# Kernel optimization log

Hardware: AMD Instinct MI355X
Metric: run time of the kernel (lower is better)

## Reference

```python
import jax, jax.numpy as jnp
import numpy as np

B, S, HID = 1, 2048, 4096
N_HEADS, N_KV_HEADS, HEAD_DIM = 32, 8, 128
ROPE_THETA = 10000.0


def rotate_half(x):
    # standard Llama rotate_half along last dim
    d = x.shape[-1] // 2
    return jnp.concatenate([-x[..., d:], x[..., :d]], axis=-1)


def rope_cos_sin(position_ids, dtype):
    # inv_freq: [head_dim/2]
    inv_freq = 1.0 / (ROPE_THETA ** (jnp.arange(0, HEAD_DIM, 2, dtype=jnp.float32) / HEAD_DIM))
    freqs = position_ids.astype(jnp.float32)[:, :, None] * inv_freq[None, None, :]  # [B,S,hd/2]
    emb = jnp.concatenate([freqs, freqs], axis=-1)  # [B,S,hd]
    return jnp.cos(emb).astype(dtype), jnp.sin(emb).astype(dtype)


def setup_inputs() -> dict:
    key = jax.random.key(0)
    ks = jax.random.split(key, 5)
    scale = 0.02
    return {
        "hidden_states": jax.random.normal(ks[0], (B, S, HID), dtype=jnp.float32),
        "position_ids": jnp.broadcast_to(jnp.arange(S, dtype=jnp.int32)[None, :], (B, S)),
        "Wq": jax.random.normal(ks[1], (N_HEADS * HEAD_DIM, HID), dtype=jnp.float32) * scale,
        "Wk": jax.random.normal(ks[2], (N_KV_HEADS * HEAD_DIM, HID), dtype=jnp.float32) * scale,
        "Wv": jax.random.normal(ks[3], (N_KV_HEADS * HEAD_DIM, HID), dtype=jnp.float32) * scale,
        "Wo": jax.random.normal(ks[4], (HID, HID), dtype=jnp.float32) * scale,
    }


def reference(hidden_states, position_ids, Wq, Wk, Wv, Wo):
    bsz, q_len, _ = hidden_states.shape
    n_rep = N_HEADS // N_KV_HEADS

    # projections (torch Linear: x @ W.T)
    q = (hidden_states @ Wq.T).reshape(bsz, q_len, N_HEADS, HEAD_DIM).transpose(0, 2, 1, 3)
    k = (hidden_states @ Wk.T).reshape(bsz, q_len, N_KV_HEADS, HEAD_DIM).transpose(0, 2, 1, 3)
    v = (hidden_states @ Wv.T).reshape(bsz, q_len, N_KV_HEADS, HEAD_DIM).transpose(0, 2, 1, 3)

    cos, sin = rope_cos_sin(position_ids, hidden_states.dtype)
    cos = cos[:, None, :, :]  # [B,1,S,hd]
    sin = sin[:, None, :, :]
    q = q * cos + rotate_half(q) * sin
    k = k * cos + rotate_half(k) * sin

    # GQA: repeat kv heads
    k = jnp.repeat(k, n_rep, axis=1)  # [B,nH,S,hd]
    v = jnp.repeat(v, n_rep, axis=1)

    scores = jnp.einsum("bhqd,bhkd->bhqk", q, k) / jnp.sqrt(jnp.asarray(HEAD_DIM, q.dtype))
    causal = jnp.tril(jnp.ones((q_len, q_len), dtype=bool))
    neg = jnp.asarray(jnp.finfo(jnp.float32).min, scores.dtype)
    scores = jnp.where(causal[None, None, :, :], scores, neg)

    attn = jax.nn.softmax(scores.astype(jnp.float32), axis=-1).astype(q.dtype)
    out = jnp.einsum("bhqk,bhkd->bhqd", attn, v)  # [B,nH,S,hd]
    out = out.transpose(0, 2, 1, 3).reshape(bsz, q_len, HID)
    return out @ Wo.T
```

## Files before the change

kernel.cpp:

```cpp
#include <hip/hip_runtime.h>

typedef __attribute__((ext_vector_type(4))) float f32x4;
typedef __attribute__((ext_vector_type(8))) __bf16 bf16x8;
typedef __attribute__((ext_vector_type(4))) unsigned short u16x4;

#define DEVI static __device__ __forceinline__
#define AS1 __attribute__((address_space(1)))
#define AS3 __attribute__((address_space(3)))

static constexpr int S_LEN = 2048;
static constexpr int HID   = 4096;
static constexpr int NH    = 32;
static constexpr int NKV   = 8;
static constexpr int HD    = 128;
static constexpr int NQKV  = HID + 2 * NKV * HD;

DEVI unsigned short f2bf(float f) {
  unsigned int u = __float_as_uint(f);
  u += 0x7FFFu + ((u >> 16) & 1u);
  return (unsigned short)(u >> 16);
}
DEVI float bf2f(unsigned short h) {
  return __uint_as_float(((unsigned int)h) << 16);
}

__global__ void cast_f32_bf16(const float* __restrict__ in,
                              unsigned short* __restrict__ out, int n4) {
  int i = blockIdx.x * 256 + threadIdx.x;
  if (i >= n4) return;
  float4 v = reinterpret_cast<const float4*>(in)[i];
  u16x4 o;
  o[0] = f2bf(v.x); o[1] = f2bf(v.y); o[2] = f2bf(v.z); o[3] = f2bf(v.w);
  reinterpret_cast<u16x4*>(out)[i] = o;
}

__global__ void cast_all(const float* __restrict__ hs,
                         const float* __restrict__ Wq,
                         const float* __restrict__ Wk,
                         const float* __restrict__ Wv,
                         unsigned short* __restrict__ H16,
                         unsigned short* __restrict__ Wcat) {
  const int nH  = S_LEN * HID / 4;
  const int nWq = HID * HID / 4;
  const int nWkv = NKV * HD * HID / 4;
  int i = blockIdx.x * 256 + threadIdx.x;
  const float* src; unsigned short* dst; int idx;
  if (i < nH)                    { src = hs; dst = H16; idx = i; }
  else if (i < nH + nWq)         { src = Wq; dst = Wcat; idx = i - nH; }
  else if (i < nH + nWq + nWkv)  { src = Wk; dst = Wcat + (size_t)HID * HID; idx = i - nH - nWq; }
  else                           { src = Wv; dst = Wcat + (size_t)(HID + NKV * HD) * HID;
                                   idx = i - nH - nWq - nWkv; }
  float4 v = reinterpret_cast<const float4*>(src)[idx];
  u16x4 o;
  o[0] = f2bf(v.x); o[1] = f2bf(v.y); o[2] = f2bf(v.z); o[3] = f2bf(v.w);
  reinterpret_cast<u16x4*>(dst)[idx] = o;
}

__global__ void rope_table(float2* __restrict__ tab) {
  int i = blockIdx.x * 256 + threadIdx.x;
  if (i >= S_LEN * 64) return;
  int j = i & 63, s = i >> 6;
  float inv = powf(10000.0f, -(float)j / 64.0f);
  float ang = (float)s * inv;
  tab[i] = make_float2(cosf(ang), sinf(ang));
}

__global__ void rope_all(unsigned short* __restrict__ Qb,
                         unsigned short* __restrict__ Kb,
                         const float2* __restrict__ tab) {
  const int totq = S_LEN * NH * 64;
  const int tot  = totq + S_LEN * NKV * 64;
  int i = blockIdx.x * 256 + threadIdx.x;
  if (i >= tot) return;
  unsigned short* X; int Hn, idx;
  if (i < totq) { X = Qb; Hn = NH; idx = i; }
  else          { X = Kb; Hn = NKV; idx = i - totq; }
  int j = idx & 63;
  int h = (idx >> 6) % Hn;
  int s = idx / (64 * Hn);
  float2 cs = tab[s * 64 + j];
  unsigned short* p = X + (size_t)s * Hn * HD + h * HD;
  float x1 = bf2f(p[j]);
  float x2 = bf2f(p[j + 64]);
  p[j]      = f2bf(x1 * cs.x - x2 * cs.y);
  p[j + 64] = f2bf(x2 * cs.x + x1 * cs.y);
}

__global__ __launch_bounds__(256, 2) void gemm_qkv_h(
    const unsigned short* __restrict__ A,
    const unsigned short* __restrict__ B,
    unsigned short* __restrict__ Qb,
    unsigned short* __restrict__ Kb,
    unsigned short* __restrict__ Vt) {
  __shared__ __align__(16) unsigned short lds[2][20480];
  const int tid = threadIdx.x;
  const int lane = tid & 63, w = tid >> 6;
  const int wm = w >> 1, wn = w & 1;
  const int lr = lane & 15, lg = lane >> 4;
  const int n0 = blockIdx.x * 192, m0 = blockIdx.y * 128;
  const int Kd = HID;

  const int sAr = tid >> 3, sAp = tid & 7;
  auto stA = [&](int buf, int t, int u) {
    int row = u * 32 + sAr;
    __builtin_amdgcn_global_load_lds(
        (const AS1 void*)(A + (size_t)(m0 + row) * Kd + t * 64 + ((sAp ^ (row & 7)) * 8)),
        (AS3 void*)(&lds[buf][row * 64 + sAp * 8]), 16, 0, 0);
  };
  auto stB = [&](int buf, int t, int v) {
    int row = v * 32 + sAr;
    __builtin_amdgcn_global_load_lds(
        (const AS1 void*)(B + (size_t)(n0 + row) * Kd + t * 64 + ((sAp ^ (row & 7)) * 8)),
        (AS3 void*)(&lds[buf][8192 + row * 64 + sAp * 8]), 16, 0, 0);
  };

  const int arow = (wm * 64 + lr) * 64;
  const int brow = 8192 + (wn * 96 + lr) * 64;
  const int ck0 = (lg ^ (lr & 7)) * 8;
  const int ck1 = ((4 + lg) ^ (lr & 7)) * 8;

  f32x4 acc[4][6] = {};
  bf16x8 bgr[6];

#pragma unroll
  for (int u = 0; u < 4; ++u) { stA(0, 0, u); stA(1, 1, u); }
#pragma unroll
  for (int v = 0; v < 6; ++v) { stB(0, 0, v); stB(1, 1, v); }
  asm volatile("s_waitcnt vmcnt(0)" ::: "memory");
  __builtin_amdgcn_s_barrier();

#define QPHASE(BUF, KH, MH, LOADB, WAITOP, ...)                                \
  do {                                                                         \
    const int ck = (KH) ? ck1 : ck0;                                           \
    const unsigned short* ab = &lds[BUF][arow + (MH) * 2048 + ck];             \
    bf16x8 af0 = *reinterpret_cast<const bf16x8*>(ab);                         \
    bf16x8 af1 = *reinterpret_cast<const bf16x8*>(ab + 1024);                  \
    if (LOADB) {                                                               \
      const unsigned short* bb = &lds[BUF][brow + ck];                         \
      bgr[0] = *reinterpret_cast<const bf16x8*>(bb);                           \
      bgr[1] = *reinterpret_cast<const bf16x8*>(bb + 1024);                    \
      bgr[2] = *reinterpret_cast<const bf16x8*>(bb + 2048);                    \
      bgr[3] = *reinterpret_cast<const bf16x8*>(bb + 3072);                    \
      bgr[4] = *reinterpret_cast<const bf16x8*>(bb + 4096);                    \
      bgr[5] = *reinterpret_cast<const bf16x8*>(bb + 5120);                    \
    }                                                                          \
    __builtin_amdgcn_sched_barrier(0);                                         \
    __VA_ARGS__                                                                \
    WAITOP                                                                     \
    __builtin_amdgcn_s_barrier();                                              \
    asm volatile("s_waitcnt lgkmcnt(0)" ::: "memory");                         \
    __builtin_amdgcn_sched_barrier(0);                                         \
    __builtin_amdgcn_s_setprio(1);                                             \
    acc[(MH)*2+0][0] = __builtin_amdgcn_mfma_f32_16x16x32_bf16(af0, bgr[0], acc[(MH)*2+0][0],0,0,0); \
    acc[(MH)*2+0][1] = __builtin_amdgcn_mfma_f32_16x16x32_bf16(af0, bgr[1], acc[(MH)*2+0][1],0,0,0); \
    acc[(MH)*2+0][2] = __builtin_amdgcn_mfma_f32_16x16x32_bf16(af0, bgr[2], acc[(MH)*2+0][2],0,0,0); \
    acc[(MH)*2+0][3] = __builtin_amdgcn_mfma_f32_16x16x32_bf16(af0, bgr[3], acc[(MH)*2+0][3],0,0,0); \
    acc[(MH)*2+0][4] = __builtin_amdgcn_mfma_f32_16x16x32_bf16(af0, bgr[4], acc[(MH)*2+0][4],0,0,0); \
    acc[(MH)*2+0][5] = __builtin_amdgcn_mfma_f32_16x16x32_bf16(af0, bgr[5], acc[(MH)*2+0][5],0,0,0); \
    acc[(MH)*2+1][0] = __builtin_amdgcn_mfma_f32_16x16x32_bf16(af1, bgr[0], acc[(MH)*2+1][0],0,0,0); \
    acc[(MH)*2+1][1] = __builtin_amdgcn_mfma_f32_16x16x32_bf16(af1, bgr[1], acc[(MH)*2+1][1],0,0,0); \
    acc[(MH)*2+1][2] = __builtin_amdgcn_mfma_f32_16x16x32_bf16(af1, bgr[2], acc[(MH)*2+1][2],0,0,0); \
    acc[(MH)*2+1][3] = __builtin_amdgcn_mfma_f32_16x16x32_bf16(af1, bgr[3], acc[(MH)*2+1][3],0,0,0); \
    acc[(MH)*2+1][4] = __builtin_amdgcn_mfma_f32_16x16x32_bf16(af1, bgr[4], acc[(MH)*2+1][4],0,0,0); \
    acc[(MH)*2+1][5] = __builtin_amdgcn_mfma_f32_16x16x32_bf16(af1, bgr[5], acc[(MH)*2+1][5],0,0,0); \
    __builtin_amdgcn_s_setprio(0);                                             \
    __builtin_amdgcn_s_barrier();                                              \
  } while (0)

#define QVM0 asm volatile("s_waitcnt vmcnt(0)" ::: "memory");
#define QNOW

  for (int i = 0; i < 32; ++i) {
    const int t = 2 * i;
    const bool nf = (i != 0), nl = (i != 31);
    QPHASE(0, 0, 0, 1, QNOW, if (nf) { stA(1, t + 1, 0); stA(1, t + 1, 1);
                                       stA(1, t + 1, 2); stA(1, t + 1, 3);
                                       stB(1, t + 1, 0); stB(1, t + 1, 1); stB(1, t + 1, 2);
                                       stB(1, t + 1, 3); stB(1, t + 1, 4); stB(1, t + 1, 5); });
    QPHASE(0, 0, 1, 0, QNOW, ;);
    QPHASE(0, 1, 0, 1, QNOW, ;);
    QPHASE(0, 1, 1, 0, QVM0, ;);
    QPHASE(1, 0, 0, 1, QNOW, if (nl) { stA(0, t + 2, 0); stA(0, t + 2, 1);
                                       stA(0, t + 2, 2); stA(0, t + 2, 3);
                                       stB(0, t + 2, 0); stB(0, t + 2, 1); stB(0, t + 2, 2);
                                       stB(0, t + 2, 3); stB(0, t + 2, 4); stB(0, t + 2, 5); });
    QPHASE(1, 0, 1, 0, QNOW, ;);
    QPHASE(1, 1, 0, 1, QNOW, ;);
    QPHASE(1, 1, 1, 0, QVM0, ;);
  }
#undef QPHASE
#undef QVM0
#undef QNOW

#pragma unroll
  for (int ar = 0; ar < 4; ++ar) {
#pragma unroll
    for (int c = 0; c < 6; ++c) {
      const int gcolb = n0 + wn * 96 + c * 16;
      const int gcol = gcolb + lr;
      const int growb = m0 + wm * 64 + ar * 16 + lg * 4;
      if (gcolb < HID) {
#pragma unroll
        for (int rr = 0; rr < 4; ++rr)
          Qb[(size_t)(growb + rr) * HID + gcol] = f2bf(acc[ar][c][rr]);
      } else if (gcolb < HID + NKV * HD) {
#pragma unroll
        for (int rr = 0; rr < 4; ++rr)
          Kb[(size_t)(growb + rr) * (NKV * HD) + (gcol - HID)] = f2bf(acc[ar][c][rr]);
      } else {
        u16x4 o4;
#pragma unroll
        for (int rr = 0; rr < 4; ++rr) o4[rr] = f2bf(acc[ar][c][rr]);
        *reinterpret_cast<u16x4*>(
            &Vt[(size_t)(gcol - HID - NKV * HD) * S_LEN + growb]) = o4;
      }
    }
  }
}

__global__ __launch_bounds__(512, 2) void gemm_o256(
    const unsigned short* __restrict__ A,
    const unsigned short* __restrict__ B,
    float* __restrict__ C) {
  __shared__ __align__(16) unsigned short lds[2][24576];
  const int tid = threadIdx.x;
  const int lane = tid & 63, w = tid >> 6;
  const int wm = w >> 2, wn = w & 3;
  const int lr = lane & 15, lg = lane >> 4;
  const int m0 = blockIdx.y * 128, n0 = blockIdx.x * 256;
  const int Kd = HID;

  const int sAr = tid >> 3, sAp = tid & 7;
  const int sBn = tid >> 2, sBp = tid & 3;
  auto stA = [&](int buf, int t, int unit) {
    int row = unit * 64 + sAr;
    __builtin_amdgcn_global_load_lds(
        (const AS1 void*)(A + (size_t)(m0 + row) * Kd + t * 64 + ((sAp ^ (row & 7)) * 8)),
        (AS3 void*)(&lds[buf][row * 64 + sAp * 8]), 16, 0, 0);
  };
  auto stB = [&](int buf, int t, int kh, int hb) {
    int n = hb * 128 + sBn;
    __builtin_amdgcn_global_load_lds(
        (const AS1 void*)(B + (size_t)(n0 + n) * Kd + t * 64 + kh * 32 + ((sBp ^ ((n >> 1) & 3)) * 8)),
        (AS3 void*)(&lds[buf][8192 + kh * 8192 + n * 32 + sBp * 8]), 16, 0, 0);
  };

  const int aoffk0 = (wm * 64 + lr) * 64 + ((lg ^ (lr & 7)) * 8);
  const int aoffk1 = (wm * 64 + lr) * 64 + (((4 + lg) ^ (lr & 7)) * 8);
  const int boff   = 8192 + (wn * 64 + lr) * 32 + ((lg ^ ((lr >> 1) & 3)) * 8);

  f32x4 acc[4][4] = {};
  bf16x8 bgr[4];

#pragma unroll
  for (int u = 0; u < 2; ++u) { stA(0, 0, u); stA(1, 1, u); }
#pragma unroll
  for (int kh = 0; kh < 2; ++kh)
#pragma unroll
    for (int hb = 0; hb < 2; ++hb) { stB(0, 0, kh, hb); stB(1, 1, kh, hb); }
  asm volatile("s_waitcnt vmcnt(0)" ::: "memory");
  __builtin_amdgcn_s_barrier();

#define OPHASE(BUF, KH, MH, LOADB, WAITOP, ...)                                \
  do {                                                                         \
    const unsigned short* ab = &lds[BUF][((KH) ? aoffk1 : aoffk0) + (MH) * 2048];\
    bf16x8 af0 = *reinterpret_cast<const bf16x8*>(ab);                         \
    bf16x8 af1 = *reinterpret_cast<const bf16x8*>(ab + 1024);                  \
    if (LOADB) {                                                               \
      const unsigned short* bb = &lds[BUF][boff + (KH) * 8192];                \
      bgr[0] = *reinterpret_cast<const bf16x8*>(bb);                           \
      bgr[1] = *reinterpret_cast<const bf16x8*>(bb + 512);                     \
      bgr[2] = *reinterpret_cast<const bf16x8*>(bb + 1024);                    \
      bgr[3] = *reinterpret_cast<const bf16x8*>(bb + 1536);                    \
    }                                                                          \
    __builtin_amdgcn_sched_barrier(0);                                         \
    __VA_ARGS__                                                                \
    WAITOP                                                                     \
    __builtin_amdgcn_s_barrier();                                              \
    asm volatile("s_waitcnt lgkmcnt(0)" ::: "memory");                         \
    __builtin_amdgcn_sched_barrier(0);                                         \
    __builtin_amdgcn_s_setprio(1);                                             \
    acc[(MH)*2+0][0] = __builtin_amdgcn_mfma_f32_16x16x32_bf16(af0, bgr[0], acc[(MH)*2+0][0],0,0,0); \
    acc[(MH)*2+0][1] = __builtin_amdgcn_mfma_f32_16x16x32_bf16(af0, bgr[1], acc[(MH)*2+0][1],0,0,0); \
    acc[(MH)*2+0][2] = __builtin_amdgcn_mfma_f32_16x16x32_bf16(af0, bgr[2], acc[(MH)*2+0][2],0,0,0); \
    acc[(MH)*2+0][3] = __builtin_amdgcn_mfma_f32_16x16x32_bf16(af0, bgr[3], acc[(MH)*2+0][3],0,0,0); \
    acc[(MH)*2+1][0] = __builtin_amdgcn_mfma_f32_16x16x32_bf16(af1, bgr[0], acc[(MH)*2+1][0],0,0,0); \
    acc[(MH)*2+1][1] = __builtin_amdgcn_mfma_f32_16x16x32_bf16(af1, bgr[1], acc[(MH)*2+1][1],0,0,0); \
    acc[(MH)*2+1][2] = __builtin_amdgcn_mfma_f32_16x16x32_bf16(af1, bgr[2], acc[(MH)*2+1][2],0,0,0); \
    acc[(MH)*2+1][3] = __builtin_amdgcn_mfma_f32_16x16x32_bf16(af1, bgr[3], acc[(MH)*2+1][3],0,0,0); \
    __builtin_amdgcn_s_setprio(0);                                             \
    __builtin_amdgcn_s_barrier();                                              \
  } while (0)

#define VM2 asm volatile("s_waitcnt vmcnt(2)" ::: "memory");
#define VM0 asm volatile("s_waitcnt vmcnt(0)" ::: "memory");
#define NOW

  for (int i = 0; i < 31; ++i) {
    const int t = 2 * i;
    const bool nf = (i != 0);
    OPHASE(0, 0, 0, 1, NOW, if (nf) { stA(1, t + 1, 0); stA(1, t + 1, 1);
                                      stB(1, t + 1, 1, 0); stB(1, t + 1, 1, 1); });
    OPHASE(0, 0, 1, 0, NOW, ;);
    OPHASE(0, 1, 0, 1, NOW, { stB(0, t + 2, 0, 0); stB(0, t + 2, 0, 1); });
    OPHASE(0, 1, 1, 0, VM2, ;);
    OPHASE(1, 0, 0, 1, NOW, { stA(0, t + 2, 0); stA(0, t + 2, 1);
                              stB(0, t + 2, 1, 0); stB(0, t + 2, 1, 1); });
    OPHASE(1, 0, 1, 0, NOW, ;);
    OPHASE(1, 1, 0, 1, NOW, { stB(1, t + 3, 0, 0); stB(1, t + 3, 0, 1); });
    OPHASE(1, 1, 1, 0, VM2, ;);
  }
  {
    const int t = 62;
    OPHASE(0, 0, 0, 1, NOW, { stA(1, t + 1, 0); stA(1, t + 1, 1);
                              stB(1, t + 1, 1, 0); stB(1, t + 1, 1, 1); });
    OPHASE(0, 0, 1, 0, NOW, ;);
    OPHASE(0, 1, 0, 1, NOW, ;);
    OPHASE(0, 1, 1, 0, VM0, ;);
    OPHASE(1, 0, 0, 1, NOW, ;);
    OPHASE(1, 0, 1, 0, NOW, ;);
    OPHASE(1, 1, 0, 1, NOW, ;);
    OPHASE(1, 1, 1, 0, NOW, ;);
  }
#undef OPHASE
#undef VM2
#undef VM0
#undef NOW

#pragma unroll
  for (int ar = 0; ar < 4; ++ar) {
#pragma unroll
    for (int fc = 0; fc < 4; ++fc) {
      const int gcol = n0 + wn * 64 + fc * 16 + lr;
      const int growb = m0 + wm * 64 + ar * 16 + lg * 4;
#pragma unroll
      for (int rr = 0; rr < 4; ++rr)
        C[(size_t)(growb + rr) * HID + gcol] = acc[ar][fc][rr];
    }
  }
}

__global__ __launch_bounds__(512, 4) void attn_kernel(
    const unsigned short* __restrict__ Q,
    const unsigned short* __restrict__ Kb,
    const unsigned short* __restrict__ Vt,
    unsigned short* __restrict__ O) {
  __shared__ __align__(16) unsigned short sK[2][64 * 128];
  __shared__ __align__(16) unsigned short sV[2][128 * 64];
  const int tid = threadIdx.x;
  const int lane = tid & 63, w = tid >> 6;
  const int lr = lane & 15, lg = lane >> 4;
  const int b = blockIdx.x;
  const int half = b >> 8, u = b & 255;
  const int h = u & 31, kvh = (u & 31) >> 2;
  const int j = u >> 5;
  const int qt = half ? (15 - j) : j;
  const int q0 = qt * 128, qw = q0 + w * 16;
  const int KVS = NKV * HD;

  bf16x8 qf[4];
#pragma unroll
  for (int ks = 0; ks < 4; ++ks)
    qf[ks] = *reinterpret_cast<const bf16x8*>(
        &Q[(size_t)(qw + lr) * HID + h * HD + ks * 32 + lg * 8]);

  f32x4 ao[8] = {};
  float mrun = -INFINITY, lrun = 0.f;
  const float S2 = 0.12751745f;
  const int ntiles = 2 * qt + 2;

  auto stage = [&](int bb, int kv0) {
#pragma unroll
    for (int i = 0; i < 2; ++i) {
      int off = (tid + i * 512) * 8;
      int r = off >> 7, c = (off >> 3) & 15;
      __builtin_amdgcn_global_load_lds(
          (const AS1 void*)(Kb + (size_t)(kv0 + r) * KVS + kvh * HD + ((c ^ (r & 15)) * 8)),
          (AS3 void*)(&sK[bb][off]), 16, 0, 0);
    }
#pragma unroll
    for (int i = 0; i < 2; ++i) {
      int off = (tid + i * 512) * 8;
      int r = off >> 6, c = (off >> 3) & 7;
      __builtin_amdgcn_global_load_lds(
          (const AS1 void*)(Vt + (size_t)(kvh * HD + r) * S_LEN + kv0 + ((c ^ (r & 7)) * 8)),
          (AS3 void*)(&sV[bb][off]), 16, 0, 0);
    }
  };

  stage(0, 0);
  __syncthreads();
  int cur = 0;

  for (int t = 0; t < ntiles; ++t) {
    const int kv0 = t * 64;
    if (t + 1 < ntiles) stage(cur ^ 1, kv0 + 64);

    if (kv0 <= qw + 15) {
      f32x4 sacc[4] = {};
      __builtin_amdgcn_s_setprio(1);
#pragma unroll
      for (int kt = 0; kt < 4; ++kt)
#pragma unroll
        for (int ks = 0; ks < 4; ++ks) {
          int elem = (kt * 16 + lr) * 128 + (((4 * ks + lg) ^ lr) * 8);
          bf16x8 kf = *reinterpret_cast<const bf16x8*>(&sK[cur][elem]);
          sacc[kt] = __builtin_amdgcn_mfma_f32_16x16x32_bf16(kf, qf[ks], sacc[kt], 0, 0, 0);
        }
      __builtin_amdgcn_s_setprio(0);

      const bool needMask = (kv0 + 63 > qw);
      const int qg = qw + lr;
      float p[16];
      float tmax = -INFINITY;
#pragma unroll
      for (int kt = 0; kt < 4; ++kt)
#pragma unroll
        for (int r = 0; r < 4; ++r) {
          float v = sacc[kt][r] * S2;
          if (needMask && (kv0 + kt * 16 + lg * 4 + r > qg)) v = -INFINITY;
          p[kt * 4 + r] = v;
          tmax = fmaxf(tmax, v);
        }
      tmax = fmaxf(tmax, __shfl_xor(tmax, 16));
      tmax = fmaxf(tmax, __shfl_xor(tmax, 32));
      if (!__all(tmax <= mrun + 8.0f)) {
        float mnew = fmaxf(mrun, tmax);
        float corr = exp2f(mrun - mnew);
        lrun *= corr;
#pragma unroll
        for (int dt = 0; dt < 8; ++dt) ao[dt] *= corr;
        mrun = mnew;
      }
      float rs = 0.f;
#pragma unroll
      for (int i = 0; i < 16; ++i) { p[i] = exp2f(p[i] - mrun); rs += p[i]; }
      rs += __shfl_xor(rs, 16);
      rs += __shfl_xor(rs, 32);
      lrun += rs;

      unsigned int bfrag[2][4];
#pragma unroll
      for (int g = 0; g < 2; ++g) {
        unsigned int Au = (unsigned)f2bf(p[8 * g + 0]) | ((unsigned)f2bf(p[8 * g + 1]) << 16);
        unsigned int Bu = (unsigned)f2bf(p[8 * g + 2]) | ((unsigned)f2bf(p[8 * g + 3]) << 16);
        unsigned int Cu = (unsigned)f2bf(p[8 * g + 4]) | ((unsigned)f2bf(p[8 * g + 5]) << 16);
        unsigned int Du = (unsigned)f2bf(p[8 * g + 6]) | ((unsigned)f2bf(p[8 * g + 7]) << 16);
        int s0 = (lg & 1) * 2;
        int src0 = lr + 16 * s0, src1 = src0 + 16;
        bool hi = lg >= 2;
        int a0 = __shfl((int)Au, src0), c0 = __shfl((int)Cu, src0);
        int b0 = __shfl((int)Bu, src0), d0 = __shfl((int)Du, src0);
        int a1 = __shfl((int)Au, src1), c1 = __shfl((int)Cu, src1);
        int b1 = __shfl((int)Bu, src1), d1 = __shfl((int)Du, src1);
        bfrag[g][0] = hi ? (unsigned)c0 : (unsigned)a0;
        bfrag[g][1] = hi ? (unsigned)d0 : (unsigned)b0;
        bfrag[g][2] = hi ? (unsigned)c1 : (unsigned)a1;
        bfrag[g][3] = hi ? (unsigned)d1 : (unsigned)b1;
      }

      __builtin_amdgcn_s_setprio(1);
#pragma unroll
      for (int g = 0; g < 2; ++g)
#pragma unroll
        for (int dt = 0; dt < 8; ++dt) {
          int d = dt * 16 + lr;
          int elem = d * 64 + (((4 * g + lg) ^ (lr & 7)) * 8);
          bf16x8 vf = *reinterpret_cast<const bf16x8*>(&sV[cur][elem]);
          ao[dt] = __builtin_amdgcn_mfma_f32_16x16x32_bf16(
              vf, *reinterpret_cast<const bf16x8*>(&bfrag[g]), ao[dt], 0, 0, 0);
        }
      __builtin_amdgcn_s_setprio(0);
    }

    __syncthreads();
    cur ^= 1;
  }

  float inv = 1.0f / lrun;
  int qrow = qw + lr;
#pragma unroll
  for (int dt = 0; dt < 8; ++dt) {
    u16x4 o4;
#pragma unroll
    for (int r = 0; r < 4; ++r) o4[r] = f2bf(ao[dt][r] * inv);
    *reinterpret_cast<u16x4*>(&O[(size_t)qrow * HID + h * HD + dt * 16 + lg * 4]) = o4;
  }
}

extern "C" void kernel_launch(void* const* d_in, const int* in_sizes, int n_in,
                              void* d_out, int out_size, void* d_ws, size_t ws_size,
                              hipStream_t stream) {
  const float* hs = (const float*)d_in[0];
  const float* Wq = (const float*)d_in[2];
  const float* Wk = (const float*)d_in[3];
  const float* Wv = (const float*)d_in[4];
  const float* Wo = (const float*)d_in[5];

  unsigned short* ws = (unsigned short*)d_ws;
  size_t off = 0;
  unsigned short* H16  = ws + off; off += (size_t)S_LEN * HID;
  unsigned short* Wcat = ws + off; off += (size_t)NQKV * HID;
  unsigned short* Qb   = ws + off; off += (size_t)S_LEN * HID;
  unsigned short* Kb   = ws + off; off += (size_t)S_LEN * NKV * HD;
  unsigned short* Vt   = ws + off; off += (size_t)S_LEN * NKV * HD;
  float2* tab = (float2*)(ws + off); off += (size_t)S_LEN * 64 * 2 * 2;

  rope_table<<<(S_LEN * 64 + 255) / 256, 256, 0, stream>>>(tab);

  {
    int n4 = (S_LEN * HID + HID * HID + 2 * NKV * HD * HID) / 4;
    cast_all<<<(n4 + 255) / 256, 256, 0, stream>>>(hs, Wq, Wk, Wv, H16, Wcat);
  }

  gemm_qkv_h<<<dim3(NQKV / 192, S_LEN / 128), 256, 0, stream>>>(
      H16, Wcat, Qb, Kb, Vt);

  {
    int n4 = HID * HID / 4;
    cast_f32_bf16<<<(n4 + 255) / 256, 256, 0, stream>>>(Wo, Wcat, n4);
  }

  {
    int tot = S_LEN * NH * 64 + S_LEN * NKV * 64;
    rope_all<<<(tot + 255) / 256, 256, 0, stream>>>(Qb, Kb, tab);
  }

  attn_kernel<<<dim3(512), 512, 0, stream>>>(Qb, Kb, Vt, H16);

  gemm_o256<<<dim3(HID / 256, S_LEN / 128), 512, 0, stream>>>(
      H16, Wcat, (float*)d_out);
}
```

Baseline: 316.2 us.

## Process two query sub-tiles per attention wave, grid-stride cast and vectorized rope

The attention kernel drops to 256 threads per block, and each wave now handles 32 query rows as two 16-row sub-tiles. Each K fragment read from LDS is reused for two MFMAs and each V fragment for two, which halves LDS traffic per MFMA but roughly doubles accumulator registers per wave. The cast kernels and the rope kernel become grid-stride loops with fixed grid sizes. The rope kernel also processes four elements per thread with vectorized loads, cutting launch overhead and per-element address arithmetic.

```diff
diff --git a/kernel.cpp b/kernel.cpp
--- a/kernel.cpp
+++ b/kernel.cpp
@@ -26,12 +26,12 @@
 
 __global__ void cast_f32_bf16(const float* __restrict__ in,
                               unsigned short* __restrict__ out, int n4) {
-  int i = blockIdx.x * 256 + threadIdx.x;
-  if (i >= n4) return;
-  float4 v = reinterpret_cast<const float4*>(in)[i];
-  u16x4 o;
-  o[0] = f2bf(v.x); o[1] = f2bf(v.y); o[2] = f2bf(v.z); o[3] = f2bf(v.w);
-  reinterpret_cast<u16x4*>(out)[i] = o;
+  for (int i = blockIdx.x * 256 + threadIdx.x; i < n4; i += gridDim.x * 256) {
+    float4 v = reinterpret_cast<const float4*>(in)[i];
+    u16x4 o;
+    o[0] = f2bf(v.x); o[1] = f2bf(v.y); o[2] = f2bf(v.z); o[3] = f2bf(v.w);
+    reinterpret_cast<u16x4*>(out)[i] = o;
+  }
 }
 
 __global__ void cast_all(const float* __restrict__ hs,
@@ -43,17 +43,19 @@
   const int nH  = S_LEN * HID / 4;
   const int nWq = HID * HID / 4;
   const int nWkv = NKV * HD * HID / 4;
-  int i = blockIdx.x * 256 + threadIdx.x;
-  const float* src; unsigned short* dst; int idx;
-  if (i < nH)                    { src = hs; dst = H16; idx = i; }
-  else if (i < nH + nWq)         { src = Wq; dst = Wcat; idx = i - nH; }
-  else if (i < nH + nWq + nWkv)  { src = Wk; dst = Wcat + (size_t)HID * HID; idx = i - nH - nWq; }
-  else                           { src = Wv; dst = Wcat + (size_t)(HID + NKV * HD) * HID;
-                                   idx = i - nH - nWq - nWkv; }
-  float4 v = reinterpret_cast<const float4*>(src)[idx];
-  u16x4 o;
-  o[0] = f2bf(v.x); o[1] = f2bf(v.y); o[2] = f2bf(v.z); o[3] = f2bf(v.w);
-  reinterpret_cast<u16x4*>(dst)[idx] = o;
+  const int tot = nH + nWq + 2 * nWkv;
+  for (int i = blockIdx.x * 256 + threadIdx.x; i < tot; i += gridDim.x * 256) {
+    const float* src; unsigned short* dst; int idx;
+    if (i < nH)                    { src = hs; dst = H16; idx = i; }
+    else if (i < nH + nWq)         { src = Wq; dst = Wcat; idx = i - nH; }
+    else if (i < nH + nWq + nWkv)  { src = Wk; dst = Wcat + (size_t)HID * HID; idx = i - nH - nWq; }
+    else                           { src = Wv; dst = Wcat + (size_t)(HID + NKV * HD) * HID;
+                                     idx = i - nH - nWq - nWkv; }
+    float4 v = reinterpret_cast<const float4*>(src)[idx];
+    u16x4 o;
+    o[0] = f2bf(v.x); o[1] = f2bf(v.y); o[2] = f2bf(v.z); o[3] = f2bf(v.w);
+    reinterpret_cast<u16x4*>(dst)[idx] = o;
+  }
 }
 
 __global__ void rope_table(float2* __restrict__ tab) {
@@ -68,22 +70,29 @@
 __global__ void rope_all(unsigned short* __restrict__ Qb,
                          unsigned short* __restrict__ Kb,
                          const float2* __restrict__ tab) {
-  const int totq = S_LEN * NH * 64;
-  const int tot  = totq + S_LEN * NKV * 64;
-  int i = blockIdx.x * 256 + threadIdx.x;
-  if (i >= tot) return;
-  unsigned short* X; int Hn, idx;
-  if (i < totq) { X = Qb; Hn = NH; idx = i; }
-  else          { X = Kb; Hn = NKV; idx = i - totq; }
-  int j = idx & 63;
-  int h = (idx >> 6) % Hn;
-  int s = idx / (64 * Hn);
-  float2 cs = tab[s * 64 + j];
-  unsigned short* p = X + (size_t)s * Hn * HD + h * HD;
-  float x1 = bf2f(p[j]);
-  float x2 = bf2f(p[j + 64]);
-  p[j]      = f2bf(x1 * cs.x - x2 * cs.y);
-  p[j + 64] = f2bf(x2 * cs.x + x1 * cs.y);
+  const int totq = S_LEN * NH * 16;
+  const int tot  = totq + S_LEN * NKV * 16;
+  for (int i = blockIdx.x * 256 + threadIdx.x; i < tot; i += gridDim.x * 256) {
+    unsigned short* X; int Hn, idx;
+    if (i < totq) { X = Qb; Hn = NH; idx = i; }
+    else          { X = Kb; Hn = NKV; idx = i - totq; }
+    int j4 = idx & 15;
+    int h  = (idx >> 4) % Hn;
+    int s  = idx / (16 * Hn);
+    unsigned short* p = X + (size_t)s * Hn * HD + h * HD + j4 * 4;
+    u16x4 lo = *reinterpret_cast<u16x4*>(p);
+    u16x4 hi = *reinterpret_cast<u16x4*>(p + 64);
+    u16x4 olo, ohi;
+#pragma unroll
+    for (int k = 0; k < 4; ++k) {
+      float2 cs = tab[s * 64 + j4 * 4 + k];
+      float x1 = bf2f(lo[k]), x2 = bf2f(hi[k]);
+      olo[k] = f2bf(x1 * cs.x - x2 * cs.y);
+      ohi[k] = f2bf(x2 * cs.x + x1 * cs.y);
+    }
+    *reinterpret_cast<u16x4*>(p) = olo;
+    *reinterpret_cast<u16x4*>(p + 64) = ohi;
+  }
 }
 
 __global__ __launch_bounds__(256, 2) void gemm_qkv_h(
@@ -340,7 +349,7 @@
   }
 }
 
-__global__ __launch_bounds__(512, 4) void attn_kernel(
+__global__ __launch_bounds__(256, 2) void attn_kernel(
     const unsigned short* __restrict__ Q,
     const unsigned short* __restrict__ Kb,
     const unsigned short* __restrict__ Vt,
@@ -355,32 +364,35 @@
   const int h = u & 31, kvh = (u & 31) >> 2;
   const int j = u >> 5;
   const int qt = half ? (15 - j) : j;
-  const int q0 = qt * 128, qw = q0 + w * 16;
+  const int q0 = qt * 128, qw = q0 + w * 32;
   const int KVS = NKV * HD;
 
-  bf16x8 qf[4];
-#pragma unroll
-  for (int ks = 0; ks < 4; ++ks)
-    qf[ks] = *reinterpret_cast<const bf16x8*>(
-        &Q[(size_t)(qw + lr) * HID + h * HD + ks * 32 + lg * 8]);
-
-  f32x4 ao[8] = {};
-  float mrun = -INFINITY, lrun = 0.f;
+  bf16x8 qf[2][4];
+#pragma unroll
+  for (int q2 = 0; q2 < 2; ++q2)
+#pragma unroll
+    for (int ks = 0; ks < 4; ++ks)
+      qf[q2][ks] = *reinterpret_cast<const bf16x8*>(
+          &Q[(size_t)(qw + q2 * 16 + lr) * HID + h * HD + ks * 32 + lg * 8]);
+
+  f32x4 ao[2][8] = {};
+  float mrun[2] = {-INFINITY, -INFINITY};
+  float lrun[2] = {0.f, 0.f};
   const float S2 = 0.12751745f;
   const int ntiles = 2 * qt + 2;
 
   auto stage = [&](int bb, int kv0) {
 #pragma unroll
-    for (int i = 0; i < 2; ++i) {
-      int off = (tid + i * 512) * 8;
+    for (int i = 0; i < 4; ++i) {
+      int off = (tid + i * 256) * 8;
       int r = off >> 7, c = (off >> 3) & 15;
       __builtin_amdgcn_global_load_lds(
           (const AS1 void*)(Kb + (size_t)(kv0 + r) * KVS + kvh * HD + ((c ^ (r & 15)) * 8)),
           (AS3 void*)(&sK[bb][off]), 16, 0, 0);
     }
 #pragma unroll
-    for (int i = 0; i < 2; ++i) {
-      int off = (tid + i * 512) * 8;
+    for (int i = 0; i < 4; ++i) {
+      int off = (tid + i * 256) * 8;
       int r = off >> 6, c = (off >> 3) & 7;
       __builtin_amdgcn_global_load_lds(
           (const AS1 void*)(Vt + (size_t)(kvh * HD + r) * S_LEN + kv0 + ((c ^ (r & 7)) * 8)),
@@ -396,8 +408,9 @@
     const int kv0 = t * 64;
     if (t + 1 < ntiles) stage(cur ^ 1, kv0 + 64);
 
-    if (kv0 <= qw + 15) {
-      f32x4 sacc[4] = {};
+    if (kv0 <= qw + 31) {
+      const bool act0 = (kv0 <= qw + 15);
+      f32x4 sacc[2][4] = {};
       __builtin_amdgcn_s_setprio(1);
 #pragma unroll
       for (int kt = 0; kt < 4; ++kt)
@@ -405,58 +418,63 @@
         for (int ks = 0; ks < 4; ++ks) {
           int elem = (kt * 16 + lr) * 128 + (((4 * ks + lg) ^ lr) * 8);
           bf16x8 kf = *reinterpret_cast<const bf16x8*>(&sK[cur][elem]);
-          sacc[kt] = __builtin_amdgcn_mfma_f32_16x16x32_bf16(kf, qf[ks], sacc[kt], 0, 0, 0);
+          sacc[0][kt] = __builtin_amdgcn_mfma_f32_16x16x32_bf16(kf, qf[0][ks], sacc[0][kt], 0, 0, 0);
+          sacc[1][kt] = __builtin_amdgcn_mfma_f32_16x16x32_bf16(kf, qf[1][ks], sacc[1][kt], 0, 0, 0);
         }
       __builtin_amdgcn_s_setprio(0);
 
-      const bool needMask = (kv0 + 63 > qw);
-      const int qg = qw + lr;
-      float p[16];
-      float tmax = -INFINITY;
-#pragma unroll
-      for (int kt = 0; kt < 4; ++kt)
-#pragma unroll
-        for (int r = 0; r < 4; ++r) {
-          float v = sacc[kt][r] * S2;
-          if (needMask && (kv0 + kt * 16 + lg * 4 + r > qg)) v = -INFINITY;
-          p[kt * 4 + r] = v;
-          tmax = fmaxf(tmax, v);
+      unsigned int bfrag[2][2][4];
+      const bool needMask = (kv0 + 63 > qw + 16);
+#pragma unroll
+      for (int q2 = 0; q2 < 2; ++q2) {
+        if (q2 == 0 && !act0) continue;
+        const int qg = qw + q2 * 16 + lr;
+        float p[16];
+        float tmax = -INFINITY;
+#pragma unroll
+        for (int kt = 0; kt < 4; ++kt)
+#pragma unroll
+          for (int r = 0; r < 4; ++r) {
+            float v = sacc[q2][kt][r] * S2;
+            if (needMask && (kv0 + kt * 16 + lg * 4 + r > qg)) v = -INFINITY;
+            p[kt * 4 + r] = v;
+            tmax = fmaxf(tmax, v);
+          }
+        tmax = fmaxf(tmax, __shfl_xor(tmax, 16));
+        tmax = fmaxf(tmax, __shfl_xor(tmax, 32));
+        if (!__all(tmax <= mrun[q2] + 8.0f)) {
+          float mnew = fmaxf(mrun[q2], tmax);
+          float corr = exp2f(mrun[q2] - mnew);
+          lrun[q2] *= corr;
+#pragma unroll
+          for (int dt = 0; dt < 8; ++dt) ao[q2][dt] *= corr;
+          mrun[q2] = mnew;
         }
-      tmax = fmaxf(tmax, __shfl_xor(tmax, 16));
-      tmax = fmaxf(tmax, __shfl_xor(tmax, 32));
-      if (!__all(tmax <= mrun + 8.0f)) {
-        float mnew = fmaxf(mrun, tmax);
-        float corr = exp2f(mrun - mnew);
-        lrun *= corr;
-#pragma unroll
-        for (int dt = 0; dt < 8; ++dt) ao[dt] *= corr;
-        mrun = mnew;
-      }
-      float rs = 0.f;
-#pragma unroll
-      for (int i = 0; i < 16; ++i) { p[i] = exp2f(p[i] - mrun); rs += p[i]; }
-      rs += __shfl_xor(rs, 16);
-      rs += __shfl_xor(rs, 32);
-      lrun += rs;
-
-      unsigned int bfrag[2][4];
-#pragma unroll
-      for (int g = 0; g < 2; ++g) {
-        unsigned int Au = (unsigned)f2bf(p[8 * g + 0]) | ((unsigned)f2bf(p[8 * g + 1]) << 16);
-        unsigned int Bu = (unsigned)f2bf(p[8 * g + 2]) | ((unsigned)f2bf(p[8 * g + 3]) << 16);
-        unsigned int Cu = (unsigned)f2bf(p[8 * g + 4]) | ((unsigned)f2bf(p[8 * g + 5]) << 16);
-        unsigned int Du = (unsigned)f2bf(p[8 * g + 6]) | ((unsigned)f2bf(p[8 * g + 7]) << 16);
-        int s0 = (lg & 1) * 2;
-        int src0 = lr + 16 * s0, src1 = src0 + 16;
-        bool hi = lg >= 2;
-        int a0 = __shfl((int)Au, src0), c0 = __shfl((int)Cu, src0);
-        int b0 = __shfl((int)Bu, src0), d0 = __shfl((int)Du, src0);
-        int a1 = __shfl((int)Au, src1), c1 = __shfl((int)Cu, src1);
-        int b1 = __shfl((int)Bu, src1), d1 = __shfl((int)Du, src1);
-        bfrag[g][0] = hi ? (unsigned)c0 : (unsigned)a0;
-        bfrag[g][1] = hi ? (unsigned)d0 : (unsigned)b0;
-        bfrag[g][2] = hi ? (unsigned)c1 : (unsigned)a1;
-        bfrag[g][3] = hi ? (unsigned)d1 : (unsigned)b1;
+        float rs = 0.f;
+#pragma unroll
+        for (int i = 0; i < 16; ++i) { p[i] = exp2f(p[i] - mrun[q2]); rs += p[i]; }
+        rs += __shfl_xor(rs, 16);
+        rs += __shfl_xor(rs, 32);
+        lrun[q2] += rs;
+
+#pragma unroll
+        for (int g = 0; g < 2; ++g) {
+          unsigned int Au = (unsigned)f2bf(p[8 * g + 0]) | ((unsigned)f2bf(p[8 * g + 1]) << 16);
+          unsigned int Bu = (unsigned)f2bf(p[8 * g + 2]) | ((unsigned)f2bf(p[8 * g + 3]) << 16);
+          unsigned int Cu = (unsigned)f2bf(p[8 * g + 4]) | ((unsigned)f2bf(p[8 * g + 5]) << 16);
+          unsigned int Du = (unsigned)f2bf(p[8 * g + 6]) | ((unsigned)f2bf(p[8 * g + 7]) << 16);
+          int s0 = (lg & 1) * 2;
+          int src0 = lr + 16 * s0, src1 = src0 + 16;
+          bool hi = lg >= 2;
+          int a0 = __shfl((int)Au, src0), c0 = __shfl((int)Cu, src0);
+          int b0 = __shfl((int)Bu, src0), d0 = __shfl((int)Du, src0);
+          int a1 = __shfl((int)Au, src1), c1 = __shfl((int)Cu, src1);
+          int b1 = __shfl((int)Bu, src1), d1 = __shfl((int)Du, src1);
+          bfrag[q2][g][0] = hi ? (unsigned)c0 : (unsigned)a0;
+          bfrag[q2][g][1] = hi ? (unsigned)d0 : (unsigned)b0;
+          bfrag[q2][g][2] = hi ? (unsigned)c1 : (unsigned)a1;
+          bfrag[q2][g][3] = hi ? (unsigned)d1 : (unsigned)b1;
+        }
       }
 
       __builtin_amdgcn_s_setprio(1);
@@ -467,8 +485,11 @@
           int d = dt * 16 + lr;
           int elem = d * 64 + (((4 * g + lg) ^ (lr & 7)) * 8);
           bf16x8 vf = *reinterpret_cast<const bf16x8*>(&sV[cur][elem]);
-          ao[dt] = __builtin_amdgcn_mfma_f32_16x16x32_bf16(
-              vf, *reinterpret_cast<const bf16x8*>(&bfrag[g]), ao[dt], 0, 0, 0);
+          if (act0)
+            ao[0][dt] = __builtin_amdgcn_mfma_f32_16x16x32_bf16(
+                vf, *reinterpret_cast<const bf16x8*>(&bfrag[0][g]), ao[0][dt], 0, 0, 0);
+          ao[1][dt] = __builtin_amdgcn_mfma_f32_16x16x32_bf16(
+              vf, *reinterpret_cast<const bf16x8*>(&bfrag[1][g]), ao[1][dt], 0, 0, 0);
         }
       __builtin_amdgcn_s_setprio(0);
     }
@@ -477,14 +498,17 @@
     cur ^= 1;
   }
 
-  float inv = 1.0f / lrun;
-  int qrow = qw + lr;
-#pragma unroll
-  for (int dt = 0; dt < 8; ++dt) {
-    u16x4 o4;
-#pragma unroll
-    for (int r = 0; r < 4; ++r) o4[r] = f2bf(ao[dt][r] * inv);
-    *reinterpret_cast<u16x4*>(&O[(size_t)qrow * HID + h * HD + dt * 16 + lg * 4]) = o4;
+#pragma unroll
+  for (int q2 = 0; q2 < 2; ++q2) {
+    float inv = 1.0f / lrun[q2];
+    int qrow = qw + q2 * 16 + lr;
+#pragma unroll
+    for (int dt = 0; dt < 8; ++dt) {
+      u16x4 o4;
+#pragma unroll
+      for (int r = 0; r < 4; ++r) o4[r] = f2bf(ao[q2][dt][r] * inv);
+      *reinterpret_cast<u16x4*>(&O[(size_t)qrow * HID + h * HD + dt * 16 + lg * 4]) = o4;
+    }
   }
 }
 
@@ -508,25 +532,16 @@
 
   rope_table<<<(S_LEN * 64 + 255) / 256, 256, 0, stream>>>(tab);
 
-  {
-    int n4 = (S_LEN * HID + HID * HID + 2 * NKV * HD * HID) / 4;
-    cast_all<<<(n4 + 255) / 256, 256, 0, stream>>>(hs, Wq, Wk, Wv, H16, Wcat);
-  }
+  cast_all<<<2048, 256, 0, stream>>>(hs, Wq, Wk, Wv, H16, Wcat);
 
   gemm_qkv_h<<<dim3(NQKV / 192, S_LEN / 128), 256, 0, stream>>>(
       H16, Wcat, Qb, Kb, Vt);
 
-  {
-    int n4 = HID * HID / 4;
-    cast_f32_bf16<<<(n4 + 255) / 256, 256, 0, stream>>>(Wo, Wcat, n4);
-  }
-
-  {
-    int tot = S_LEN * NH * 64 + S_LEN * NKV * 64;
-    rope_all<<<(tot + 255) / 256, 256, 0, stream>>>(Qb, Kb, tab);
-  }
-
-  attn_kernel<<<dim3(512), 512, 0, stream>>>(Qb, Kb, Vt, H16);
+  cast_f32_bf16<<<1024, 256, 0, stream>>>(Wo, Wcat, HID * HID / 4);
+
+  rope_all<<<2048, 256, 0, stream>>>(Qb, Kb, tab);
+
+  attn_kernel<<<dim3(512), 256, 0, stream>>>(Qb, Kb, Vt, H16);
 
   gemm_o256<<<dim3(HID / 256, S_LEN / 128), 512, 0, stream>>>(
       H16, Wcat, (float*)d_out);
```

Result: slower. 335.8 us (+6.2%).
